# Performance work log

Measured on AMD Instinct MI355X. Metric: run time of the kernel, lower is better.

The kernel has to match this reference:

```python
import jax, jax.numpy as jnp
import numpy as np

HEADS = 2


def _log_cpb(h, w, w1, b1, w2):
    # Swin-v2 style continuous relative position bias on an h*w grid.
    yy, xx = jnp.meshgrid(jnp.arange(h), jnp.arange(w), indexing='ij')
    coords = jnp.stack([yy.reshape(-1), xx.reshape(-1)], axis=-1).astype(jnp.float32)  # (L, 2)
    rel = coords[:, None, :] - coords[None, :, :]                                      # (L, L, 2)
    denom = jnp.array([max(h - 1, 1), max(w - 1, 1)], dtype=jnp.float32)
    rel = rel / denom * 8.0
    rel = jnp.sign(rel) * jnp.log2(1.0 + jnp.abs(rel)) / np.float32(np.log2(8.0))
    bias = jax.nn.relu(rel @ w1.T + b1) @ w2.T                                         # (L, L, heads)
    return jnp.transpose(bias, (2, 0, 1))                                              # (heads, L, L)


def setup_inputs() -> dict:
    key = jax.random.key(0)
    ks = jax.random.split(key, 11)
    b, s, c, h, w = 2, 32, 128, 24, 24
    hid, out_ch = 256, 128
    sc = lambda n: 1.0 / np.sqrt(n)
    return {
        'x':      jax.random.normal(ks[0], (b, s, c, h, w), jnp.float32),
        'qk_w':   jax.random.normal(ks[1], (2 * c, c), jnp.float32) * sc(c),
        'v_w':    jax.random.normal(ks[2], (hid, c), jnp.float32) * sc(c),
        'cpb_w1': jax.random.normal(ks[3], (c, 2), jnp.float32) * sc(2),
        'cpb_b1': jax.random.normal(ks[4], (c,), jnp.float32) * 0.02,
        'cpb_w2': jax.random.normal(ks[5], (HEADS, c), jnp.float32) * sc(c),
        'sa_bias': jax.random.uniform(ks[6], (hid, 1, 1), jnp.float32, -sc(c), sc(c)),
        'mlp_w1': jax.random.normal(ks[7], (hid, hid), jnp.float32) * sc(hid),
        'mlp_b1': jax.random.normal(ks[8], (hid,), jnp.float32) * 0.02,
        'mlp_w2': jax.random.normal(ks[9], (out_ch, hid), jnp.float32) * sc(hid),
        'mlp_b2': jax.random.normal(ks[10], (out_ch,), jnp.float32) * 0.02,
    }


def reference(x, qk_w, v_w, cpb_w1, cpb_b1, cpb_w2, sa_bias, mlp_w1, mlp_b1, mlp_w2, mlp_b2):
    b, s, c, h, w = x.shape
    L = h * w
    qkd = c // HEADS
    vd = v_w.shape[0] // HEADS
    xr = x.reshape(b * s, c, L)                                        # flatten (b s) and (h w)
    # QKV via 1x1 convs == channel matmuls
    qk = jnp.einsum('oc,bcl->bol', qk_w, xr)                           # (bs, 2c, L)
    qk = qk.reshape(b * s, 2, HEADS, qkd, L).transpose(1, 0, 2, 4, 3)  # (2, bs, heads, L, d)
    q, k = qk[0], qk[1]
    v = jnp.einsum('oc,bcl->bol', v_w, xr).reshape(b * s, HEADS, vd, L).transpose(0, 1, 3, 2)
    # learned continuous relative position bias, added as SDPA attn_mask
    bias = _log_cpb(h, w, cpb_w1, cpb_b1, cpb_w2)                      # (heads, L, L)
    scale = np.float32(1.0 / np.sqrt(qkd))
    scores = jnp.einsum('bhld,bhmd->bhlm', q, k) * scale + bias[None]
    attn = jax.nn.softmax(scores, axis=-1)
    out = jnp.einsum('bhlm,bhmd->bhld', attn, v)                       # (bs, heads, L, vd)
    out = out.transpose(0, 1, 3, 2).reshape(b, s, HEADS * vd, h, w)
    out = out + sa_bias[None, None]                                    # (b, s, hid, h, w)
    # 1x1-conv MLP with exact GELU
    y = jnp.einsum('oi,bsihw->bsohw', mlp_w1, out) + mlp_b1[None, None, :, None, None]
    y = jax.nn.gelu(y, approximate=False)
    y = jnp.einsum('oi,bsihw->bsohw', mlp_w2, y) + mlp_b2[None, None, :, None, None]
    return y
```

## Files before the change

kernel.cpp:

```cpp
#include <hip/hip_runtime.h>
#include <cstdint>
#include <cstddef>

constexpr int BS   = 64;
constexpr int Cc   = 128;
constexpr int Lc   = 576;
constexpr int VD   = 128;
constexpr int HID  = 256;
constexpr int OUTC = 128;
constexpr int NPIX = BS * Lc;

typedef __bf16 bf16x8 __attribute__((ext_vector_type(8)));
typedef float  f32x4  __attribute__((ext_vector_type(4)));
typedef unsigned short u16x8 __attribute__((ext_vector_type(8)));
typedef unsigned int   u32x4 __attribute__((ext_vector_type(4)));

__device__ __forceinline__ unsigned short f2bf(float f) {
  unsigned int u = __builtin_bit_cast(unsigned int, f);
  u += 0x7fffu + ((u >> 16) & 1u);
  return (unsigned short)(u >> 16);
}
__device__ __forceinline__ float bf2f(unsigned short h) {
  unsigned int u = ((unsigned int)h) << 16;
  return __builtin_bit_cast(float, u);
}
__device__ __forceinline__ unsigned int packhl(float v) {
  unsigned short hi = f2bf(v);
  unsigned short lo = f2bf(v - bf2f(hi));
  return ((unsigned int)hi << 16) | (unsigned int)lo;
}
__device__ __forceinline__ void unpack8(u32x4 a, u32x4 b, bf16x8& hi, bf16x8& lo) {
  u32x4 h, l;
  h[0] = (a[1] & 0xffff0000u) | (a[0] >> 16);
  l[0] = (a[1] << 16)         | (a[0] & 0xffffu);
  h[1] = (a[3] & 0xffff0000u) | (a[2] >> 16);
  l[1] = (a[3] << 16)         | (a[2] & 0xffffu);
  h[2] = (b[1] & 0xffff0000u) | (b[0] >> 16);
  l[2] = (b[1] << 16)         | (b[0] & 0xffffu);
  h[3] = (b[3] & 0xffff0000u) | (b[2] >> 16);
  l[3] = (b[3] << 16)         | (b[2] & 0xffffu);
  hi = __builtin_bit_cast(bf16x8, h);
  lo = __builtin_bit_cast(bf16x8, l);
}

#define MFMA16(a, b, c) __builtin_amdgcn_mfma_f32_16x16x32_bf16((a), (b), (c), 0, 0, 0)

__global__ __launch_bounds__(256) void cpb_kernel(const float* __restrict__ w1,
                                                  const float* __restrict__ b1,
                                                  const float* __restrict__ w2,
                                                  float* __restrict__ tab) {
  int idx = blockIdx.x * 256 + threadIdx.x;
  if (idx >= 47 * 47) return;
  int dy = idx / 47 - 23, dx = idx % 47 - 23;
  float fy = (float)dy * (8.0f / 23.0f);
  float fx = (float)dx * (8.0f / 23.0f);
  fy = copysignf(log2f(1.0f + fabsf(fy)) * (1.0f / 3.0f), fy);
  fx = copysignf(log2f(1.0f + fabsf(fx)) * (1.0f / 3.0f), fx);
  float a0 = 0.f, a1 = 0.f;
  for (int hh = 0; hh < 128; hh++) {
    float hv = fmaxf(w1[2 * hh] * fy + w1[2 * hh + 1] * fx + b1[hh], 0.f);
    a0 += w2[hh] * hv;
    a1 += w2[128 + hh] * hv;
  }
  tab[idx] = a0;
  tab[2209 + idx] = a1;
}

__global__ __launch_bounds__(256) void bias_mat(const float* __restrict__ tab,
                                                unsigned short* __restrict__ biasC) {
  int id = blockIdx.x * 256 + threadIdx.x;
  if (id >= 737280) return;
  int id2 = id % 2560;
  int grp = id / 2560;
  int wave = grp & 3;
  int mt = (grp >> 2) % 36;
  int hh = grp / 144;
  int g = id2 / 512;
  int lane = (id2 >> 3) & 63;
  int k = id2 & 7;
  int e = g * 8 + k;
  unsigned short val = 0;
  if (e < 36) {
    int ln = e >> 2, r = e & 3;
    int nt = wave * 9 + ln;
    int i = mt * 16 + (lane >> 4) * 4 + r;
    int j = nt * 16 + (lane & 15);
    int yi = i / 24, xi = i - yi * 24;
    int yj = j / 24, xj = j - yj * 24;
    val = f2bf(tab[hh * 2209 + (yi - yj + 23) * 47 + (xi - xj + 23)]);
  }
  biasC[id] = val;
}

__global__ __launch_bounds__(256) void prep_w(
    const float* __restrict__ w1, const float* __restrict__ w2,
    const float* __restrict__ qkw, const float* __restrict__ vw,
    unsigned short* __restrict__ w1h, unsigned short* __restrict__ w1l,
    unsigned short* __restrict__ w2h, unsigned short* __restrict__ w2l,
    unsigned short* __restrict__ wqkh, unsigned short* __restrict__ wqkl,
    unsigned short* __restrict__ wvh, unsigned short* __restrict__ wvl) {
  int id = blockIdx.x * 256 + threadIdx.x;
  const float* src;
  unsigned short *dh, *dl;
  int off;
  if (id < 65536)       { src = w1;  dh = w1h;  dl = w1l;  off = id; }
  else if (id < 98304)  { src = w2;  dh = w2h;  dl = w2l;  off = id - 65536; }
  else if (id < 131072) { src = qkw; dh = wqkh; dl = wqkl; off = id - 98304; }
  else if (id < 163840) { src = vw;  dh = wvh;  dl = wvl;  off = id - 131072; }
  else return;
  float v = src[off];
  unsigned short hi = f2bf(v);
  dh[off] = hi;
  dl[off] = f2bf(v - bf2f(hi));
}

__global__ __launch_bounds__(256) void prep_x(const float* __restrict__ x,
                                              unsigned short* __restrict__ xph,
                                              unsigned short* __restrict__ xpl) {
  __shared__ float xt[128 * 65];
  const int l0 = blockIdx.x * 64, bs = blockIdx.y;
  const int t = threadIdx.x;
  const float* xb = x + (size_t)bs * Cc * Lc;
#pragma unroll
  for (int pass = 0; pass < 8; pass++) {
    int f = pass * 1024 + t * 4;
    int c = f >> 6, ll = f & 63;
    *(float4*)(xt + c * 65 + ll) = *(const float4*)(xb + c * Lc + l0 + ll);
  }
  __syncthreads();
  const int rowl = t >> 2, c0 = (t & 3) * 32;
  const size_t p = (size_t)bs * Lc + l0 + rowl;
  unsigned short hbuf[32], lbuf[32];
#pragma unroll
  for (int i = 0; i < 32; i++) {
    float v = xt[(c0 + i) * 65 + rowl];
    unsigned short hi = f2bf(v);
    hbuf[i] = hi;
    lbuf[i] = f2bf(v - bf2f(hi));
  }
#pragma unroll
  for (int g = 0; g < 4; g++) {
    *(u16x8*)(xph + p * 128 + c0 + g * 8) = *(u16x8*)(hbuf + g * 8);
    *(u16x8*)(xpl + p * 128 + c0 + g * 8) = *(u16x8*)(lbuf + g * 8);
  }
}

__global__ __launch_bounds__(256, 2) void qkv_mfma(
    const unsigned short* __restrict__ xh, const unsigned short* __restrict__ xl,
    const unsigned short* __restrict__ wqkh, const unsigned short* __restrict__ wqkl,
    const unsigned short* __restrict__ wvh, const unsigned short* __restrict__ wvl,
    unsigned short* __restrict__ qg, unsigned short* __restrict__ kg,
    unsigned short* __restrict__ vg) {
  __shared__ unsigned short vt[128 * 130];
  const int t = threadIdx.x;
  const int wv = t >> 6, lane = t & 63;
  const int quad = lane >> 4, cc = lane & 15;
  const int by = blockIdx.y;
  const int m0 = blockIdx.x * 128 + (wv & 1) * 64;
  const int n0 = (wv >> 1) * 64;
  const unsigned short* Wh = (by < 2) ? wqkh : wvh;
  const unsigned short* Wl = (by < 2) ? wqkl : wvl;
  const int wrow0 = (by & 1) * 128 + n0;
  f32x4 acc[4][4];
#pragma unroll
  for (int i = 0; i < 4; i++)
#pragma unroll
    for (int j = 0; j < 4; j++) acc[i][j] = (f32x4){0.f, 0.f, 0.f, 0.f};
  for (int kc = 0; kc < 4; kc++) {
    const int kb = kc * 32 + quad * 8;
    bf16x8 Ah[4], Al[4], Bh[4], Bl[4];
#pragma unroll
    for (int i = 0; i < 4; i++) {
      size_t ar = (size_t)(m0 + i * 16 + cc) * 128 + kb;
      Ah[i] = *(const bf16x8*)(xh + ar);
      Al[i] = *(const bf16x8*)(xl + ar);
      size_t br = (size_t)(wrow0 + i * 16 + cc) * 128 + kb;
      Bh[i] = *(const bf16x8*)(Wh + br);
      Bl[i] = *(const bf16x8*)(Wl + br);
    }
#pragma unroll
    for (int i = 0; i < 4; i++)
#pragma unroll
      for (int j = 0; j < 4; j++) {
        acc[i][j] = MFMA16(Ah[i], Bh[j], acc[i][j]);
        acc[i][j] = MFMA16(Al[i], Bh[j], acc[i][j]);
        acc[i][j] = MFMA16(Ah[i], Bl[j], acc[i][j]);
      }
  }
  if (by < 2) {
    const float sc = (by == 0) ? 0.125f : 1.0f;
#pragma unroll
    for (int j = 0; j < 4; j++) {
      int o = n0 + j * 16 + cc;
#pragma unroll
      for (int i = 0; i < 4; i++)
#pragma unroll
        for (int r = 0; r < 4; r++) {
          int pl = (wv & 1) * 64 + i * 16 + quad * 4 + r;
          vt[pl * 130 + o] = f2bf(acc[i][j][r] * sc);
        }
    }
    __syncthreads();
    unsigned short* dst = (by == 0) ? qg : kg;
    const int pl = t >> 1, head = t & 1;
    const int p = blockIdx.x * 128 + pl;
    const int bs = p / 576, l = p - bs * 576;
    unsigned short* drow = dst + ((size_t)(bs * 2 + head) * Lc + l) * 64;
#pragma unroll
    for (int g = 0; g < 8; g++)
      *(u16x8*)(drow + g * 8) = *(const u16x8*)(vt + pl * 130 + head * 64 + g * 8);
  } else {
    const int head = by - 2;
#pragma unroll
    for (int j = 0; j < 4; j++) {
      int d = n0 + j * 16 + cc;
#pragma unroll
      for (int i = 0; i < 4; i++)
#pragma unroll
        for (int r = 0; r < 4; r++) {
          int pl = (wv & 1) * 64 + i * 16 + quad * 4 + r;
          vt[d * 130 + pl] = f2bf(acc[i][j][r]);
        }
    }
    __syncthreads();
    const int d = t >> 1, half = (t & 1) * 64;
#pragma unroll
    for (int c8 = 0; c8 < 8; c8++) {
      int pl = half + c8 * 8;
      int p = blockIdx.x * 128 + pl;
      int bs = p / 576, l = p - bs * 576;
      *(u16x8*)(vg + ((size_t)(bs * 2 + head) * VD + d) * Lc + l) =
          *(u16x8*)(vt + d * 130 + pl);
    }
  }
}

__global__ __launch_bounds__(256, 4) void attn_kernel(
    const unsigned short* __restrict__ qg,
    const unsigned short* __restrict__ kg,
    const unsigned short* __restrict__ vg,
    const unsigned short* __restrict__ biasC,
    const float* __restrict__ sa_bias,
    unsigned int* __restrict__ aout_p) {
  constexpr int PP = 580;
  __shared__ unsigned short Pb[32 * PP];
  __shared__ float psum[4][32];
  const int pair = blockIdx.x;
  const int hh = pair & 1, bs = pair >> 1;
  const int bm = blockIdx.y;
  const int m0 = bm * 32;
  const int t = threadIdx.x;
  const int wv = t >> 6, lane = t & 63;
  const int quad = lane >> 4, c = lane & 15;
  const unsigned short* qb = qg + ((size_t)pair * Lc + m0) * 64;
  const unsigned short* kb = kg + (size_t)pair * Lc * 64;
  const unsigned short* vb = vg + (size_t)pair * VD * Lc;
  bf16x8 qa0[2], qa1[2];
#pragma unroll
  for (int mt = 0; mt < 2; mt++) {
    const unsigned short* qp = qb + (size_t)(mt * 16 + c) * 64 + quad * 8;
    qa0[mt] = *(const bf16x8*)qp;
    qa1[mt] = *(const bf16x8*)(qp + 32);
  }
  f32x4 S[2][9];
#pragma unroll
  for (int mt = 0; mt < 2; mt++) {
    const unsigned short* bbase =
        biasC + ((((size_t)hh * 36 + (bm * 2 + mt)) * 4 + wv) * 5) * 512;
#pragma unroll
    for (int g = 0; g < 5; g++) {
      u16x8 bv = *(const u16x8*)(bbase + g * 512 + lane * 8);
#pragma unroll
      for (int k = 0; k < 8; k++) {
        int e = g * 8 + k;
        if (e < 36) S[mt][e >> 2][e & 3] = bf2f(bv[k]);
      }
    }
  }
#pragma unroll
  for (int ln = 0; ln < 9; ln++) {
    int nt = wv * 9 + ln;
    const unsigned short* kp = kb + (size_t)(nt * 16 + c) * 64 + quad * 8;
    bf16x8 b0 = *(const bf16x8*)kp;
    bf16x8 b1 = *(const bf16x8*)(kp + 32);
#pragma unroll
    for (int mt = 0; mt < 2; mt++)
      S[mt][ln] = MFMA16(qa1[mt], b1, MFMA16(qa0[mt], b0, S[mt][ln]));
  }
  float sm[2][4] = {{0.f, 0.f, 0.f, 0.f}, {0.f, 0.f, 0.f, 0.f}};
#pragma unroll
  for (int mt = 0; mt < 2; mt++)
#pragma unroll
    for (int ln = 0; ln < 9; ln++)
#pragma unroll
      for (int r = 0; r < 4; r++) {
        float e = __expf(S[mt][ln][r]);
        sm[mt][r] += e;
        Pb[(mt * 16 + quad * 4 + r) * PP + (wv * 9 + ln) * 16 + c] = f2bf(e);
      }
#pragma unroll
  for (int sh = 1; sh < 16; sh <<= 1)
#pragma unroll
    for (int mt = 0; mt < 2; mt++)
#pragma unroll
      for (int r = 0; r < 4; r++) sm[mt][r] += __shfl_xor(sm[mt][r], sh);
  if (c == 0)
#pragma unroll
    for (int mt = 0; mt < 2; mt++)
#pragma unroll
      for (int r = 0; r < 4; r++)
        psum[wv][mt * 16 + quad * 4 + r] = sm[mt][r];
  __syncthreads();
  float inv[2][4];
#pragma unroll
  for (int mt = 0; mt < 2; mt++)
#pragma unroll
    for (int r = 0; r < 4; r++) {
      int row = mt * 16 + quad * 4 + r;
      inv[mt][r] =
          1.0f / (psum[0][row] + psum[1][row] + psum[2][row] + psum[3][row]);
    }
  const int nd0 = wv * 2;
  f32x4 O[2][2];
#pragma unroll
  for (int mt = 0; mt < 2; mt++)
#pragma unroll
    for (int dd = 0; dd < 2; dd++) O[mt][dd] = (f32x4){0.f, 0.f, 0.f, 0.f};
#pragma unroll
  for (int kc = 0; kc < 18; kc++) {
    bf16x8 pa[2];
#pragma unroll
    for (int mt = 0; mt < 2; mt++)
      pa[mt] = *(const bf16x8*)(Pb + (size_t)(mt * 16 + c) * PP + kc * 32 +
                                quad * 8);
#pragma unroll
    for (int dd = 0; dd < 2; dd++) {
      bf16x8 vf = *(const bf16x8*)(vb + (size_t)((nd0 + dd) * 16 + c) * Lc +
                                   kc * 32 + quad * 8);
#pragma unroll
      for (int mt = 0; mt < 2; mt++) O[mt][dd] = MFMA16(pa[mt], vf, O[mt][dd]);
    }
  }
  unsigned int* obp = aout_p + ((size_t)bs * Lc + m0) * HID + hh * 128;
#pragma unroll
  for (int dd = 0; dd < 2; dd++) {
    float sb = sa_bias[hh * 128 + (nd0 + dd) * 16 + c];
#pragma unroll
    for (int mt = 0; mt < 2; mt++)
#pragma unroll
      for (int r = 0; r < 4; r++) {
        float v = O[mt][dd][r] * inv[mt][r] + sb;
        obp[(size_t)(mt * 16 + quad * 4 + r) * HID + (nd0 + dd) * 16 + c] =
            packhl(v);
      }
  }
}

__global__ __launch_bounds__(256, 4) void mlp_fused(
    const unsigned int* __restrict__ ap,
    const unsigned short* __restrict__ w1h, const unsigned short* __restrict__ w1l,
    const float* __restrict__ b1,
    const unsigned short* __restrict__ w2h, const unsigned short* __restrict__ w2l,
    const float* __restrict__ b2, float* __restrict__ out) {
  constexpr int YP = 258;
  __shared__ unsigned short y1h[32 * YP];
  __shared__ unsigned short y1l[32 * YP];
  const int t = threadIdx.x;
  const int wv = t >> 6, lane = t & 63;
  const int quad = lane >> 4, cc = lane & 15;
  const int M0 = blockIdx.x * 32;
  {
    const int n0 = wv * 64;
    f32x4 acc[2][4];
#pragma unroll
    for (int i = 0; i < 2; i++)
#pragma unroll
      for (int j = 0; j < 4; j++) acc[i][j] = (f32x4){0.f, 0.f, 0.f, 0.f};
    for (int kc = 0; kc < 8; kc++) {
      const int kb = kc * 32 + quad * 8;
      bf16x8 Ah[2], Al[2], Bh[4], Bl[4];
#pragma unroll
      for (int i = 0; i < 2; i++) {
        const unsigned int* arow = ap + (size_t)(M0 + i * 16 + cc) * HID + kb;
        u32x4 pa = *(const u32x4*)arow;
        u32x4 pb = *(const u32x4*)(arow + 4);
        unpack8(pa, pb, Ah[i], Al[i]);
      }
#pragma unroll
      for (int j = 0; j < 4; j++) {
        size_t br = (size_t)(n0 + j * 16 + cc) * HID + kb;
        Bh[j] = *(const bf16x8*)(w1h + br);
        Bl[j] = *(const bf16x8*)(w1l + br);
      }
#pragma unroll
      for (int i = 0; i < 2; i++)
#pragma unroll
        for (int j = 0; j < 4; j++) {
          acc[i][j] = MFMA16(Ah[i], Bh[j], acc[i][j]);
          acc[i][j] = MFMA16(Al[i], Bh[j], acc[i][j]);
          acc[i][j] = MFMA16(Ah[i], Bl[j], acc[i][j]);
        }
    }
#pragma unroll
    for (int j = 0; j < 4; j++) {
      int col = n0 + j * 16 + cc;
      float bias = b1[col];
#pragma unroll
      for (int i = 0; i < 2; i++) {
#pragma unroll
        for (int r = 0; r < 4; r++) {
          int row = i * 16 + quad * 4 + r;
          float v = acc[i][j][r] + bias;
          float g = 0.5f * v * (1.0f + erff(v * 0.70710678118654752f));
          unsigned short hi = f2bf(g);
          y1h[row * YP + col] = hi;
          y1l[row * YP + col] = f2bf(g - bf2f(hi));
        }
      }
    }
  }
  __syncthreads();
  {
    const int n0 = wv * 32;
    f32x4 acc[2][2];
#pragma unroll
    for (int i = 0; i < 2; i++)
#pragma unroll
      for (int j = 0; j < 2; j++) acc[i][j] = (f32x4){0.f, 0.f, 0.f, 0.f};
    for (int kc = 0; kc < 8; kc++) {
      const int kb = kc * 32 + quad * 8;
      bf16x8 Ah[2], Al[2], Bh[2], Bl[2];
#pragma unroll
      for (int i = 0; i < 2; i++) {
        int off = (i * 16 + cc) * YP + kb;
        Ah[i] = *(const bf16x8*)(y1h + off);
        Al[i] = *(const bf16x8*)(y1l + off);
      }
#pragma unroll
      for (int j = 0; j < 2; j++) {
        size_t br = (size_t)(n0 + j * 16 + cc) * HID + kb;
        Bh[j] = *(const bf16x8*)(w2h + br);
        Bl[j] = *(const bf16x8*)(w2l + br);
      }
#pragma unroll
      for (int i = 0; i < 2; i++)
#pragma unroll
        for (int j = 0; j < 2; j++) {
          acc[i][j] = MFMA16(Ah[i], Bh[j], acc[i][j]);
          acc[i][j] = MFMA16(Al[i], Bh[j], acc[i][j]);
          acc[i][j] = MFMA16(Ah[i], Bl[j], acc[i][j]);
        }
    }
#pragma unroll
    for (int i = 0; i < 2; i++) {
      int p = M0 + i * 16 + quad * 4;
      int bs = p / Lc, l = p - bs * Lc;
#pragma unroll
      for (int j = 0; j < 2; j++) {
        int col = n0 + j * 16 + cc;
        float bias = b2[col];
        float4 v = make_float4(acc[i][j][0] + bias, acc[i][j][1] + bias,
                               acc[i][j][2] + bias, acc[i][j][3] + bias);
        *(float4*)(out + ((size_t)bs * OUTC + col) * Lc + l) = v;
      }
    }
  }
}

extern "C" void kernel_launch(void* const* d_in, const int* in_sizes, int n_in,
                              void* d_out, int out_size, void* d_ws, size_t ws_size,
                              hipStream_t stream) {
  const float* x    = (const float*)d_in[0];
  const float* qk_w = (const float*)d_in[1];
  const float* v_w  = (const float*)d_in[2];
  const float* cw1  = (const float*)d_in[3];
  const float* cb1  = (const float*)d_in[4];
  const float* cw2  = (const float*)d_in[5];
  const float* sab  = (const float*)d_in[6];
  const float* mw1  = (const float*)d_in[7];
  const float* mb1  = (const float*)d_in[8];
  const float* mw2  = (const float*)d_in[9];
  const float* mb2  = (const float*)d_in[10];
  float* out = (float*)d_out;
  char* ws = (char*)d_ws;

  float* tab = (float*)(ws);
  unsigned short* biasC  = (unsigned short*)(ws + 65536);
  unsigned short* qg     = (unsigned short*)(ws + 1572864);
  unsigned short* kg     = (unsigned short*)(ws + 11010048);
  unsigned short* vg     = (unsigned short*)(ws + 20447232);
  unsigned short* xph    = (unsigned short*)(ws + 39321600);
  unsigned short* xpl    = (unsigned short*)(ws + 48758784);
  unsigned int*   aout_p = (unsigned int*)(ws + 58195968);
  unsigned short* w1h    = (unsigned short*)(ws + 95944704);
  unsigned short* w1l    = (unsigned short*)(ws + 96075776);
  unsigned short* w2h    = (unsigned short*)(ws + 96206848);
  unsigned short* w2l    = (unsigned short*)(ws + 96272384);
  unsigned short* wqkh   = (unsigned short*)(ws + 96337920);
  unsigned short* wqkl   = (unsigned short*)(ws + 96403456);
  unsigned short* wvh    = (unsigned short*)(ws + 96468992);
  unsigned short* wvl    = (unsigned short*)(ws + 96534528);

  cpb_kernel<<<dim3(9), dim3(256), 0, stream>>>(cw1, cb1, cw2, tab);
  bias_mat<<<dim3(2880), dim3(256), 0, stream>>>(tab, biasC);
  prep_w<<<dim3(640), dim3(256), 0, stream>>>(mw1, mw2, qk_w, v_w,
                                              w1h, w1l, w2h, w2l,
                                              wqkh, wqkl, wvh, wvl);
  prep_x<<<dim3(9, 64), dim3(256), 0, stream>>>(x, xph, xpl);
  qkv_mfma<<<dim3(288, 4), dim3(256), 0, stream>>>(xph, xpl, wqkh, wqkl,
                                                   wvh, wvl, qg, kg, vg);
  attn_kernel<<<dim3(128, 18), dim3(256), 0, stream>>>(qg, kg, vg, biasC, sab,
                                                       aout_p);
  mlp_fused<<<dim3(1152), dim3(256), 0, stream>>>(aout_p, w1h, w1l, mb1,
                                                  w2h, w2l, mb2, out);
}
```

Measured before the change: 300.5 us.

## Stage MLP input tile through LDS with double-buffered async global_load_lds

The first MLP GEMM now copies the 32-row activation tile into LDS with global_load_lds, double-buffered across the 8 k-chunks and using an XOR swizzle to avoid bank conflicts. Previously each wave re-read the same A rows straight from global memory. The GELU output is stored as packed hi/lo 32-bit words in one LDS array, replacing the two separate bf16 arrays, and the second GEMM unpacks it. This removes redundant global A loads and overlaps the next chunk's load with MFMA work, at the cost of a barrier on every k-chunk.

Result: faster. 284.0 us (-5.5%).

```diff
diff --git a/kernel.cpp b/kernel.cpp
--- a/kernel.cpp
+++ b/kernel.cpp
@@ -362,83 +362,100 @@
     const float* __restrict__ b1,
     const unsigned short* __restrict__ w2h, const unsigned short* __restrict__ w2l,
     const float* __restrict__ b2, float* __restrict__ out) {
-  constexpr int YP = 258;
-  __shared__ unsigned short y1h[32 * YP];
-  __shared__ unsigned short y1l[32 * YP];
+  constexpr int YPW = 260;
+  __shared__ unsigned int lds[32 * YPW];
   const int t = threadIdx.x;
   const int wv = t >> 6, lane = t & 63;
   const int quad = lane >> 4, cc = lane & 15;
+  const int c7 = cc & 7;
   const int M0 = blockIdx.x * 32;
+
+  const unsigned int* gsrc = ap + (size_t)(M0 + 8 * wv + (lane >> 3)) * HID +
+                             (((lane & 7) ^ (lane >> 3)) << 2);
+  __builtin_amdgcn_global_load_lds(
+      (const __attribute__((address_space(1))) unsigned int*)gsrc,
+      (__attribute__((address_space(3))) unsigned int*)(&lds[wv * 256]),
+      16, 0, 0);
+
+  const int n0 = wv * 64;
+  f32x4 acc1[2][4];
+#pragma unroll
+  for (int i = 0; i < 2; i++)
+#pragma unroll
+    for (int j = 0; j < 4; j++) acc1[i][j] = (f32x4){0.f, 0.f, 0.f, 0.f};
+  for (int kc = 0; kc < 8; kc++) {
+    __syncthreads();
+    const int bufw = (kc & 1) << 10;
+    bf16x8 Ah[2], Al[2];
+#pragma unroll
+    for (int i = 0; i < 2; i++) {
+      const int row = i * 16 + cc;
+      u32x4 pa = *(const u32x4*)&lds[bufw + row * 32 + (((2 * quad) ^ c7) << 2)];
+      u32x4 pb =
+          *(const u32x4*)&lds[bufw + row * 32 + (((2 * quad + 1) ^ c7) << 2)];
+      unpack8(pa, pb, Ah[i], Al[i]);
+    }
+    if (kc < 7) {
+      __builtin_amdgcn_global_load_lds(
+          (const __attribute__((address_space(1))) unsigned int*)(gsrc +
+                                                                  (kc + 1) * 32),
+          (__attribute__((address_space(3))) unsigned int*)(
+              &lds[(((kc + 1) & 1) << 10) + wv * 256]),
+          16, 0, 0);
+    }
+    const int kb = kc * 32 + quad * 8;
+    bf16x8 Bh[4], Bl[4];
+#pragma unroll
+    for (int j = 0; j < 4; j++) {
+      size_t br = (size_t)(n0 + j * 16 + cc) * HID + kb;
+      Bh[j] = *(const bf16x8*)(w1h + br);
+      Bl[j] = *(const bf16x8*)(w1l + br);
+    }
+#pragma unroll
+    for (int i = 0; i < 2; i++)
+#pragma unroll
+      for (int j = 0; j < 4; j++) {
+        acc1[i][j] = MFMA16(Ah[i], Bh[j], acc1[i][j]);
+        acc1[i][j] = MFMA16(Al[i], Bh[j], acc1[i][j]);
+        acc1[i][j] = MFMA16(Ah[i], Bl[j], acc1[i][j]);
+      }
+  }
+  __syncthreads();
+#pragma unroll
+  for (int j = 0; j < 4; j++) {
+    int col = n0 + j * 16 + cc;
+    float bias = b1[col];
+#pragma unroll
+    for (int i = 0; i < 2; i++)
+#pragma unroll
+      for (int r = 0; r < 4; r++) {
+        int row = i * 16 + quad * 4 + r;
+        float v = acc1[i][j][r] + bias;
+        float g = 0.5f * v * (1.0f + erff(v * 0.70710678118654752f));
+        lds[row * YPW + col] = packhl(g);
+      }
+  }
+  __syncthreads();
   {
-    const int n0 = wv * 64;
-    f32x4 acc[2][4];
+    const int n2 = wv * 32;
+    f32x4 acc2[2][2];
 #pragma unroll
     for (int i = 0; i < 2; i++)
 #pragma unroll
-      for (int j = 0; j < 4; j++) acc[i][j] = (f32x4){0.f, 0.f, 0.f, 0.f};
+      for (int j = 0; j < 2; j++) acc2[i][j] = (f32x4){0.f, 0.f, 0.f, 0.f};
     for (int kc = 0; kc < 8; kc++) {
       const int kb = kc * 32 + quad * 8;
-      bf16x8 Ah[2], Al[2], Bh[4], Bl[4];
+      bf16x8 Ah[2], Al[2], Bh[2], Bl[2];
 #pragma unroll
       for (int i = 0; i < 2; i++) {
-        const unsigned int* arow = ap + (size_t)(M0 + i * 16 + cc) * HID + kb;
+        const unsigned int* arow = &lds[(i * 16 + cc) * YPW + kb];
         u32x4 pa = *(const u32x4*)arow;
         u32x4 pb = *(const u32x4*)(arow + 4);
         unpack8(pa, pb, Ah[i], Al[i]);
       }
 #pragma unroll
-      for (int j = 0; j < 4; j++) {
-        size_t br = (size_t)(n0 + j * 16 + cc) * HID + kb;
-        Bh[j] = *(const bf16x8*)(w1h + br);
-        Bl[j] = *(const bf16x8*)(w1l + br);
-      }
-#pragma unroll
-      for (int i = 0; i < 2; i++)
-#pragma unroll
-        for (int j = 0; j < 4; j++) {
-          acc[i][j] = MFMA16(Ah[i], Bh[j], acc[i][j]);
-          acc[i][j] = MFMA16(Al[i], Bh[j], acc[i][j]);
-          acc[i][j] = MFMA16(Ah[i], Bl[j], acc[i][j]);
-        }
-    }
-#pragma unroll
-    for (int j = 0; j < 4; j++) {
-      int col = n0 + j * 16 + cc;
-      float bias = b1[col];
-#pragma unroll
-      for (int i = 0; i < 2; i++) {
-#pragma unroll
-        for (int r = 0; r < 4; r++) {
-          int row = i * 16 + quad * 4 + r;
-          float v = acc[i][j][r] + bias;
-          float g = 0.5f * v * (1.0f + erff(v * 0.70710678118654752f));
-          unsigned short hi = f2bf(g);
-          y1h[row * YP + col] = hi;
-          y1l[row * YP + col] = f2bf(g - bf2f(hi));
-        }
-      }
-    }
-  }
-  __syncthreads();
-  {
-    const int n0 = wv * 32;
-    f32x4 acc[2][2];
-#pragma unroll
-    for (int i = 0; i < 2; i++)
-#pragma unroll
-      for (int j = 0; j < 2; j++) acc[i][j] = (f32x4){0.f, 0.f, 0.f, 0.f};
-    for (int kc = 0; kc < 8; kc++) {
-      const int kb = kc * 32 + quad * 8;
-      bf16x8 Ah[2], Al[2], Bh[2], Bl[2];
-#pragma unroll
-      for (int i = 0; i < 2; i++) {
-        int off = (i * 16 + cc) * YP + kb;
-        Ah[i] = *(const bf16x8*)(y1h + off);
-        Al[i] = *(const bf16x8*)(y1l + off);
-      }
-#pragma unroll
       for (int j = 0; j < 2; j++) {
-        size_t br = (size_t)(n0 + j * 16 + cc) * HID + kb;
+        size_t br = (size_t)(n2 + j * 16 + cc) * HID + kb;
         Bh[j] = *(const bf16x8*)(w2h + br);
         Bl[j] = *(const bf16x8*)(w2l + br);
       }
@@ -446,9 +463,9 @@
       for (int i = 0; i < 2; i++)
 #pragma unroll
         for (int j = 0; j < 2; j++) {
-          acc[i][j] = MFMA16(Ah[i], Bh[j], acc[i][j]);
-          acc[i][j] = MFMA16(Al[i], Bh[j], acc[i][j]);
-          acc[i][j] = MFMA16(Ah[i], Bl[j], acc[i][j]);
+          acc2[i][j] = MFMA16(Ah[i], Bh[j], acc2[i][j]);
+          acc2[i][j] = MFMA16(Al[i], Bh[j], acc2[i][j]);
+          acc2[i][j] = MFMA16(Ah[i], Bl[j], acc2[i][j]);
         }
     }
 #pragma unroll
@@ -457,10 +474,10 @@
       int bs = p / Lc, l = p - bs * Lc;
 #pragma unroll
       for (int j = 0; j < 2; j++) {
-        int col = n0 + j * 16 + cc;
+        int col = n2 + j * 16 + cc;
         float bias = b2[col];
-        float4 v = make_float4(acc[i][j][0] + bias, acc[i][j][1] + bias,
-                               acc[i][j][2] + bias, acc[i][j][3] + bias);
+        float4 v = make_float4(acc2[i][j][0] + bias, acc2[i][j][1] + bias,
+                               acc2[i][j][2] + bias, acc2[i][j][3] + bias);
         *(float4*)(out + ((size_t)bs * OUTC + col) * Lc + l) = v;
       }
     }
```
